# Kernel tuning notes

Hardware: AMD Instinct MI355X
Metric: run time of the kernel (lower is better)

Reference implementation:

```python
import math
import jax, jax.numpy as jnp
import numpy as np

SEQ, BATCH, D_MODEL, HEADS = 2048, 2, 1024, 16
D_K = D_MODEL // HEADS


def setup_inputs() -> dict:
    key = jax.random.key(0)
    ks = jax.random.split(key, 11)
    s = 1.0 / math.sqrt(D_MODEL)
    inp = {
        "q": jax.random.normal(ks[0], (SEQ, BATCH, D_MODEL), jnp.float32),
        "k": jax.random.normal(ks[1], (SEQ, BATCH, D_MODEL), jnp.float32),
        "v": jax.random.normal(ks[2], (SEQ, BATCH, D_MODEL), jnp.float32),
        "Wq": jax.random.normal(ks[3], (D_MODEL, D_MODEL), jnp.float32) * s,
        "bq": jnp.zeros((D_MODEL,), jnp.float32),
        "Wk": jax.random.normal(ks[4], (D_MODEL, D_MODEL), jnp.float32) * s,
        "bk": jnp.zeros((D_MODEL,), jnp.float32),
        "Wv": jax.random.normal(ks[5], (D_MODEL, D_MODEL), jnp.float32) * s,
        "bv": jnp.zeros((D_MODEL,), jnp.float32),
        "Wo": jax.random.normal(ks[6], (D_MODEL, D_MODEL), jnp.float32) * s,
        "bo": jnp.zeros((D_MODEL,), jnp.float32),
    }
    return inp


def _proj(x, W, b):
    # [S,B,D] @ [D, H*Dk] -> [S,B,H,Dk]
    y = jnp.einsum('sbd,de->sbe', x, W) + b
    return y.reshape(x.shape[0], x.shape[1], HEADS, D_K)


def reference(q, k, v, Wq, bq, Wk, bk, Wv, bv, Wo, bo):
    scale = 1.0 / math.sqrt(D_K)
    query = _proj(q, Wq, bq)            # [i,b,h,d]
    key_ = _proj(k, Wk, bk)             # [j,b,h,d]
    value = _proj(v, Wv, bv)            # [j,b,h,d]
    scores = jnp.einsum('ibhd,jbhd->ijbh', query, key_) * scale
    attn = jax.nn.softmax(scores, axis=1)  # softmax over key axis j (dim=1)
    x = jnp.einsum('ijbh,jbhd->ibhd', attn, value)
    x = x.reshape(SEQ, BATCH, D_MODEL)
    return jnp.einsum('sbd,de->sbe', x, Wo) + bo
```

## Files before the change

kernel.cpp:

```cpp
#include <hip/hip_runtime.h>
#include <hip/hip_bf16.h>


typedef __attribute__((ext_vector_type(8))) short bf16x8;
typedef __attribute__((ext_vector_type(4))) float f32x4;

constexpr int SEQ   = 2048;
constexpr int BATCH = 2;
constexpr int DM    = 1024;
constexpr int DK    = 64;
constexpr int MR    = SEQ * BATCH;
constexpr int SST   = BATCH * DM;
constexpr int HD    = SEQ * DK;

#define CE_SCALE 0.18033688011112042592f

__device__ __forceinline__ unsigned pkbf(float a, float b) {
    __hip_bfloat162 h = __float22bfloat162_rn(float2{a, b});
    union { __hip_bfloat162 h2; unsigned u; } cv;
    cv.h2 = h;
    return cv.u;
}

__device__ __forceinline__ f32x4 mfma16(bf16x8 a, bf16x8 b, f32x4 c) {
    return __builtin_amdgcn_mfma_f32_16x16x32_bf16(a, b, c, 0, 0, 0);
}

__device__ __forceinline__ void gl16(const unsigned short* g, unsigned short* l) {
    __builtin_amdgcn_global_load_lds(
        (const __attribute__((address_space(1))) void*)g,
        (__attribute__((address_space(3))) void*)l, 16, 0, 0);
}

__global__ __launch_bounds__(256)
void wt_prep_all(const float* __restrict__ w0, const float* __restrict__ w1,
                 const float* __restrict__ w2, const float* __restrict__ w3,
                 unsigned short* __restrict__ o0, unsigned short* __restrict__ o1,
                 unsigned short* __restrict__ o2, unsigned short* __restrict__ o3)
{
    const int z = blockIdx.z;
    const float* W = (z == 0) ? w0 : (z == 1) ? w1 : (z == 2) ? w2 : w3;
    unsigned short* Wt = (z == 0) ? o0 : (z == 1) ? o1 : (z == 2) ? o2 : o3;
    const float sc = (z == 0) ? CE_SCALE : 1.0f;

    const int t = threadIdx.x;
    const int e = blockIdx.x * 64 + (t & 63);
    const int dq = blockIdx.y * 256 + (t >> 6) * 64;
    unsigned short* orow = Wt + (size_t)e * DM + dq;
#pragma unroll
    for (int c = 0; c < 8; ++c) {
        float f[8];
#pragma unroll
        for (int j = 0; j < 8; ++j)
            f[j] = W[(size_t)(dq + c * 8 + j) * DM + e] * sc;
        uint4 u = { pkbf(f[0], f[1]), pkbf(f[2], f[3]),
                    pkbf(f[4], f[5]), pkbf(f[6], f[7]) };
        *(uint4*)(orow + c * 8) = u;
    }
}

__global__ __launch_bounds__(256)
void qkv_cast(const float* __restrict__ qa, const float* __restrict__ ka,
              const float* __restrict__ va,
              unsigned short* __restrict__ Qb, unsigned short* __restrict__ Kb,
              unsigned short* __restrict__ Vb)
{
    const int z = blockIdx.y;
    const float* src = (z == 0) ? qa : (z == 1) ? ka : va;
    unsigned short* dst = (z == 0) ? Qb : (z == 1) ? Kb : Vb;
    const size_t i = ((size_t)blockIdx.x * 256 + threadIdx.x) * 8;
    float4 f0 = *(const float4*)(src + i);
    float4 f1 = *(const float4*)(src + i + 4);
    uint4 u = { pkbf(f0.x, f0.y), pkbf(f0.z, f0.w),
                pkbf(f1.x, f1.y), pkbf(f1.z, f1.w) };
    *(uint4*)(dst + i) = u;
}

__global__ __launch_bounds__(512)
void qkv256(const unsigned short* __restrict__ Qb,
            const unsigned short* __restrict__ Kb,
            const unsigned short* __restrict__ Vb,
            const unsigned short* __restrict__ wq,
            const unsigned short* __restrict__ wk,
            const unsigned short* __restrict__ wv,
            const float* __restrict__ bq, const float* __restrict__ bk,
            const float* __restrict__ bv,
            unsigned short* __restrict__ Qh, unsigned short* __restrict__ Kh,
            unsigned short* __restrict__ Vtp)
{
    constexpr int K = 1024;
    constexpr int SLOT = 16384;
    __shared__ unsigned short smem[49152];

    const int z = blockIdx.y;
    const unsigned short* Ab = (z == 0) ? Qb : (z == 1) ? Kb : Vb;
    const unsigned short* Bt = (z == 0) ? wq : (z == 1) ? wk : wv;
    const float* bias = (z == 0) ? bq : (z == 1) ? bk : bv;
    const float bscale = (z == 0) ? CE_SCALE : 1.0f;

    const int bx = blockIdx.x;
    const int xcd = bx & 7, j64 = bx >> 3;
    const int bm = xcd * 2 + (j64 >> 2);
    const int bn = j64 & 3;

    const int tid = threadIdx.x;
    const int wave = tid >> 6, lane = tid & 63;
    const int wr = wave >> 2, wcn = wave & 3;
    const int lrow = lane & 15, g = lane >> 4;
    const int gr = lane & 15, gc = (lane >> 4) * 8;

    const unsigned short* aU0 = Ab + (size_t)(bm * 256 + wave * 32 + gr) * K + gc;
    const unsigned short* aU1 = aU0 + (size_t)16 * K;
    const unsigned short* bU0 = Bt + (size_t)(bn * 256 + wave * 32 + gr) * K + gc;
    const unsigned short* bU1 = bU0 + (size_t)16 * K;

    f32x4 acc[8][4] = {};

    auto stage = [&](int t, int slot) {
        unsigned short* As = smem + slot * SLOT;
        unsigned short* Bs = As + 8192;
        const int k0 = t * 32;
        gl16(aU0 + k0, As + (2 * wave) * 512);
        gl16(aU1 + k0, As + (2 * wave + 1) * 512);
        gl16(bU0 + k0, Bs + (2 * wave) * 512);
        gl16(bU1 + k0, Bs + (2 * wave + 1) * 512);
    };

    stage(0, 0);
    stage(1, 1);

    int bcur = 0;
#pragma unroll 1
    for (int t = 0; t < 32; ++t) {
        const unsigned short* As = smem + bcur * SLOT;
        const unsigned short* Bs = As + 8192;

        if (t < 31) { asm volatile("s_waitcnt vmcnt(4)" ::: "memory"); }
        else        { asm volatile("s_waitcnt vmcnt(0)" ::: "memory"); }
        __builtin_amdgcn_s_barrier();

        bf16x8 af[8], bfr[4];
#pragma unroll
        for (int i = 0; i < 8; ++i)
            af[i] = *(const bf16x8*)&As[(wr * 8 + i) * 512 + lane * 8];
#pragma unroll
        for (int j = 0; j < 4; ++j)
            bfr[j] = *(const bf16x8*)&Bs[(wcn * 4 + j) * 512 + lane * 8];
        asm volatile("s_waitcnt lgkmcnt(0)" ::: "memory");
        __builtin_amdgcn_sched_barrier(0);
        __builtin_amdgcn_s_barrier();

        if (t + 2 < 32) {
            int ns = bcur + 2; if (ns >= 3) ns -= 3;
            stage(t + 2, ns);
        }

        __builtin_amdgcn_s_setprio(1);
#pragma unroll
        for (int i = 0; i < 8; ++i)
#pragma unroll
            for (int j = 0; j < 4; ++j)
                acc[i][j] = mfma16(af[i], bfr[j], acc[i][j]);
        __builtin_amdgcn_s_setprio(0);

        bcur = (bcur + 1 == 3) ? 0 : bcur + 1;
    }

    constexpr int LBS = 258;
    __syncthreads();
#pragma unroll 1
    for (int rq = 0; rq < 4; ++rq) {
        if (wr == (rq >> 1)) {
            const int i0 = (rq & 1) * 4;
#pragma unroll
            for (int j = 0; j < 4; ++j) {
                const int c = wcn * 64 + j * 16 + lrow;
                const float bb = bias[bn * 256 + c] * bscale;
#pragma unroll
                for (int i2 = 0; i2 < 4; ++i2)
#pragma unroll
                    for (int r = 0; r < 4; ++r) {
                        const int lr = i2 * 16 + 4 * g + r;
                        smem[lr * LBS + c] =
                            (unsigned short)(pkbf(acc[i0 + i2][j][r] + bb, 0.f) & 0xffffu);
                    }
            }
        }
        __syncthreads();
        if (z != 2) {
            unsigned short* C = (z == 0) ? Qh : Kh;
            const int lr = tid >> 3, ch = (tid >> 1) & 3, hf = tid & 1;
            const int grow = bm * 256 + rq * 64 + lr;
            const int s = grow >> 1, b = grow & 1, h = bn * 4 + ch;
            const unsigned short* src = &smem[lr * LBS + ch * 64 + hf * 32];
            unsigned short* dst = C + (size_t)(b * 16 + h) * HD + (size_t)s * 64 + hf * 32;
#pragma unroll
            for (int w2 = 0; w2 < 4; ++w2)
                *(uint4*)(dst + w2 * 8) = *(const uint4*)(src + w2 * 8);
        } else {
            const int ch = tid >> 7, d = (tid >> 1) & 63, b = tid & 1;
            const int h = bn * 4 + ch;
            unsigned tmp[16];
#pragma unroll
            for (int m = 0; m < 16; ++m) {
                const int p0 = 2 * m, p1 = p0 + 1;
                const int r5a = ((p0 >> 2) & 1) * 16 + (p0 >> 3) * 4 + (p0 & 3);
                const int r5b = ((p1 >> 2) & 1) * 16 + (p1 >> 3) * 4 + (p1 & 3);
                const unsigned va  = smem[(2 * r5a + b) * LBS + ch * 64 + d];
                const unsigned vb2 = smem[(2 * r5b + b) * LBS + ch * 64 + d];
                tmp[m] = va | (vb2 << 16);
            }
            const int sbase = bm * 128 + rq * 32;
            const int st = sbase >> 6, kc = (sbase >> 5) & 1;
            unsigned short* dst = Vtp + (size_t)(b * 16 + h) * HD + (size_t)d * SEQ
                                      + st * 64 + kc * 32;
#pragma unroll
            for (int w2 = 0; w2 < 4; ++w2) {
                uint4 u = { tmp[4 * w2], tmp[4 * w2 + 1], tmp[4 * w2 + 2], tmp[4 * w2 + 3] };
                *(uint4*)(dst + w2 * 8) = u;
            }
        }
        __syncthreads();
    }
}

__global__ __launch_bounds__(256)
void attn_mfma(const unsigned short* __restrict__ Qh,
               const unsigned short* __restrict__ Kh,
               const unsigned short* __restrict__ Vtp,
               unsigned short* __restrict__ Xp)
{
    __shared__ unsigned short lds[24576];

    const int tid = threadIdx.x;
    const int fid = blockIdx.x;
    const int xcd = fid & 7, idx = fid >> 3;
    const int bh = xcd * 4 + (idx >> 4);
    const int qt = idx & 15;

    const int wave = tid >> 6, lane = tid & 63;
    const int lrow = lane & 15, g = lane >> 4;
    const int s7 = lrow & 7;
    const int q0w = qt * 128 + wave * 32;

    const unsigned short* qb = Qh + (size_t)bh * HD;
    const unsigned short* kb = Kh + (size_t)bh * HD;
    const unsigned short* vb = Vtp + (size_t)bh * HD;

    const int r8 = lane >> 3, c8 = lane & 7;
    const unsigned short* ksrcA = kb + (size_t)(wave * 16 + r8) * 64 + (c8 ^ r8) * 8;
    const unsigned short* ksrcB = ksrcA + 8 * 64;
    const unsigned short* vsrcA = vb + (size_t)(wave * 16 + r8) * SEQ + (c8 ^ r8) * 8;
    const unsigned short* vsrcB = vsrcA + 8 * SEQ;

    auto stage = [&](int t, unsigned short* base) {
        const size_t ko = (size_t)t * 4096;
        const size_t vo = (size_t)t * 64;
        gl16(ksrcA + ko, base + wave * 1024);
        gl16(ksrcB + ko, base + wave * 1024 + 512);
        gl16(vsrcA + vo, base + 4096 + wave * 1024);
        gl16(vsrcB + vo, base + 4096 + wave * 1024 + 512);
    };

    bf16x8 bq[2][2];
#pragma unroll
    for (int qi = 0; qi < 2; ++qi)
#pragma unroll
        for (int dc = 0; dc < 2; ++dc)
            bq[qi][dc] = *(const bf16x8*)(qb + (size_t)(q0w + qi * 16 + lrow) * 64
                                             + dc * 32 + g * 8);

    bf16x8 aones;
    {
        union { uint4 u; bf16x8 v; } cv;
        const unsigned o2 = (lrow == 0) ? 0x3F803F80u : 0u;
        cv.u = make_uint4(o2, o2, o2, o2);
        aones = cv.v;
    }

    f32x4 oacc[4][2] = {};
    f32x4 lacc[2] = {};

    const int off0 = lrow * 64 + ((g ^ s7) * 8);
    const int off1 = lrow * 64 + (((4 + g) ^ s7) * 8);

    stage(0, lds);
    stage(1, lds + 8192);

    int bcur = 0;
#pragma unroll 1
    for (int t = 0; t < 32; ++t) {
        unsigned short* kbuf = lds + bcur * 8192;
        unsigned short* vbuf = kbuf + 4096;

        if (t < 31) { asm volatile("s_waitcnt vmcnt(4)" ::: "memory"); }
        else        { asm volatile("s_waitcnt vmcnt(0)" ::: "memory"); }
        __builtin_amdgcn_s_barrier();

        bf16x8 ak[4][2], av[4][2];
#pragma unroll
        for (int kt = 0; kt < 4; ++kt) {
            ak[kt][0] = *(const bf16x8*)(kbuf + kt * 1024 + off0);
            ak[kt][1] = *(const bf16x8*)(kbuf + kt * 1024 + off1);
        }
#pragma unroll
        for (int dt = 0; dt < 4; ++dt) {
            av[dt][0] = *(const bf16x8*)(vbuf + dt * 1024 + off0);
            av[dt][1] = *(const bf16x8*)(vbuf + dt * 1024 + off1);
        }
        asm volatile("s_waitcnt lgkmcnt(0)" ::: "memory");
        __builtin_amdgcn_sched_barrier(0);
        __builtin_amdgcn_s_barrier();

        if (t + 2 < 32) {
            int bn3 = bcur + 2; if (bn3 >= 3) bn3 -= 3;
            stage(t + 2, lds + bn3 * 8192);
        }

        uint4 pbu[2][2];
        __builtin_amdgcn_s_setprio(1);
#pragma unroll
        for (int qi = 0; qi < 2; ++qi) {
#pragma unroll
            for (int kt = 0; kt < 4; ++kt) {
                f32x4 s = { 0.f, 0.f, 0.f, 0.f };
                s = mfma16(ak[kt][0], bq[qi][0], s);
                s = mfma16(ak[kt][1], bq[qi][1], s);
                const float p0 = __builtin_amdgcn_exp2f(s[0]);
                const float p1 = __builtin_amdgcn_exp2f(s[1]);
                const float p2 = __builtin_amdgcn_exp2f(s[2]);
                const float p3 = __builtin_amdgcn_exp2f(s[3]);
                const unsigned lo = pkbf(p0, p1);
                const unsigned hi = pkbf(p2, p3);
                if (kt & 1) { pbu[kt >> 1][qi].z = lo; pbu[kt >> 1][qi].w = hi; }
                else        { pbu[kt >> 1][qi].x = lo; pbu[kt >> 1][qi].y = hi; }
            }
        }

#pragma unroll
        for (int kc = 0; kc < 2; ++kc) {
#pragma unroll
            for (int dt = 0; dt < 4; ++dt)
#pragma unroll
                for (int qi = 0; qi < 2; ++qi) {
                    union { uint4 u; bf16x8 v; } cv;
                    cv.u = pbu[kc][qi];
                    oacc[dt][qi] = mfma16(av[dt][kc], cv.v, oacc[dt][qi]);
                }
#pragma unroll
            for (int qi = 0; qi < 2; ++qi) {
                union { uint4 u; bf16x8 v; } cv;
                cv.u = pbu[kc][qi];
                lacc[qi] = mfma16(aones, cv.v, lacc[qi]);
            }
        }
        __builtin_amdgcn_s_setprio(0);

        bcur = (bcur + 1 == 3) ? 0 : bcur + 1;
    }

    const float ls0 = __shfl(lacc[0][0], lrow);
    const float ls1 = __shfl(lacc[1][0], lrow);
    const float inv0 = 1.0f / ls0, inv1 = 1.0f / ls1;

    __builtin_amdgcn_s_barrier();

    unsigned short (*osh)[72] = (unsigned short (*)[72])(lds + wave * 32 * 72);
#pragma unroll
    for (int qi = 0; qi < 2; ++qi) {
        const float inv = qi ? inv1 : inv0;
#pragma unroll
        for (int dt = 0; dt < 4; ++dt) {
            const int d0 = dt * 16 + 4 * g;
            const unsigned u0 = pkbf(oacc[dt][qi][0] * inv, oacc[dt][qi][1] * inv);
            const unsigned u1 = pkbf(oacc[dt][qi][2] * inv, oacc[dt][qi][3] * inv);
            *(unsigned*)&osh[qi * 16 + lrow][d0] = u0;
            *(unsigned*)&osh[qi * 16 + lrow][d0 + 2] = u1;
        }
    }
    const int ql = lane >> 1;
    const int dh = (lane & 1) * 32;
    unsigned short* xrow = Xp + (size_t)(q0w + ql) * SST + bh * 64 + dh;
#pragma unroll
    for (int c = 0; c < 4; ++c) {
        uint4 vv = *(const uint4*)&osh[ql][dh + c * 8];
        *(uint4*)(xrow + c * 8) = vv;
    }
}

__global__ __launch_bounds__(256)
void gemm_out(const unsigned short* __restrict__ Xp,
              const unsigned short* __restrict__ WtO,
              const float* __restrict__ bias, float* __restrict__ out)
{
    constexpr int K = 1024, N = 1024;
    __shared__ unsigned short smem[12288];
    unsigned short* As0 = smem;
    unsigned short* As1 = smem + 4096;
    unsigned short* Bs0 = smem + 8192;
    unsigned short* Bs1 = smem + 10240;

    const int l = blockIdx.x + 16 * blockIdx.y;
    const int xcd = l & 7, jj0 = l >> 3;
    const int bm = xcd * 4 + (jj0 >> 4);
    const int bn = jj0 & 15;

    const int tid = threadIdx.x;
    const int wave = tid >> 6, lane = tid & 63;
    const int wr = wave >> 1, wc = wave & 1;
    const int lrow = lane & 15, g = lane >> 4;
    const int gr = lane & 15, gc = (lane >> 4) * 8;

    const unsigned short* aRow0 = Xp + (size_t)(bm * 128 + wave * 32 + gr) * K + gc;
    const unsigned short* aRow1 = aRow0 + (size_t)16 * K;
    const unsigned short* bRow0 = WtO + (size_t)(bn * 64 + wave * 16 + gr) * K + gc;

    f32x4 acc[4][2] = {};

    auto stage0 = [&](int k0) {
        gl16(aRow0 + k0, As0 + (2 * wave) * 512);
        gl16(aRow1 + k0, As0 + (2 * wave + 1) * 512);
        gl16(bRow0 + k0, Bs0 + wave * 512);
    };
    auto stage1 = [&](int k0) {
        gl16(aRow0 + k0, As1 + (2 * wave) * 512);
        gl16(aRow1 + k0, As1 + (2 * wave + 1) * 512);
        gl16(bRow0 + k0, Bs1 + wave * 512);
    };
    auto loadFrag = [&](bf16x8 (&af)[4], bf16x8 (&bfr)[2],
                        const unsigned short* as, const unsigned short* bs) {
#pragma unroll
        for (int i = 0; i < 4; ++i)
            af[i] = *(const bf16x8*)&as[(wr * 4 + i) * 512 + lane * 8];
#pragma unroll
        for (int j = 0; j < 2; ++j)
            bfr[j] = *(const bf16x8*)&bs[(wc * 2 + j) * 512 + lane * 8];
    };
    auto domfma = [&](bf16x8 (&af)[4], bf16x8 (&bfr)[2]) {
        __builtin_amdgcn_s_setprio(1);
#pragma unroll
        for (int i = 0; i < 4; ++i)
#pragma unroll
            for (int j = 0; j < 2; ++j)
                acc[i][j] = mfma16(af[i], bfr[j], acc[i][j]);
        __builtin_amdgcn_s_setprio(0);
    };

    stage0(0);
    stage1(32);

#pragma unroll 1
    for (int k0 = 0; k0 < 960; k0 += 64) {
        asm volatile("s_waitcnt vmcnt(3)" ::: "memory");
        __builtin_amdgcn_s_barrier();
        {
            bf16x8 af[4], bfr[2];
            loadFrag(af, bfr, As0, Bs0);
            asm volatile("s_waitcnt lgkmcnt(0)" ::: "memory");
            __builtin_amdgcn_sched_barrier(0);
            __builtin_amdgcn_s_barrier();
            stage0(k0 + 64);
            domfma(af, bfr);
        }
        asm volatile("s_waitcnt vmcnt(3)" ::: "memory");
        __builtin_amdgcn_s_barrier();
        {
            bf16x8 af[4], bfr[2];
            loadFrag(af, bfr, As1, Bs1);
            asm volatile("s_waitcnt lgkmcnt(0)" ::: "memory");
            __builtin_amdgcn_sched_barrier(0);
            __builtin_amdgcn_s_barrier();
            stage1(k0 + 96);
            domfma(af, bfr);
        }
    }
    {
        asm volatile("s_waitcnt vmcnt(3)" ::: "memory");
        __builtin_amdgcn_s_barrier();
        bf16x8 af[4], bfr[2];
        loadFrag(af, bfr, As0, Bs0);
        domfma(af, bfr);
    }
    {
        asm volatile("s_waitcnt vmcnt(0)" ::: "memory");
        __builtin_amdgcn_s_barrier();
        bf16x8 af[4], bfr[2];
        loadFrag(af, bfr, As1, Bs1);
        domfma(af, bfr);
    }

    __syncthreads();
    float* LF = (float*)smem;
#pragma unroll 1
    for (int q2 = 0; q2 < 2; ++q2) {
        if (wr == q2) {
#pragma unroll
            for (int j = 0; j < 2; ++j) {
                const int c = wc * 32 + j * 16 + lrow;
                const float bb = bias[bn * 64 + c];
#pragma unroll
                for (int i = 0; i < 4; ++i)
#pragma unroll
                    for (int r = 0; r < 4; ++r)
                        LF[(i * 16 + 4 * g + r) * 68 + c] = acc[i][j][r] + bb;
            }
        }
        __syncthreads();
        {
            const int lr = tid >> 2, c0 = (tid & 3) * 16;
            const float* srcp = &LF[lr * 68 + c0];
            float* dst = out + (size_t)(bm * 128 + q2 * 64 + lr) * N + bn * 64 + c0;
#pragma unroll
            for (int w2 = 0; w2 < 4; ++w2)
                *(float4*)(dst + w2 * 4) = *(const float4*)(srcp + w2 * 4);
        }
        __syncthreads();
    }
}

extern "C" void kernel_launch(void* const* d_in, const int* in_sizes, int n_in,
                              void* d_out, int out_size, void* d_ws, size_t ws_size,
                              hipStream_t stream) {
    (void)in_sizes; (void)n_in; (void)out_size; (void)ws_size;

    const float* q  = (const float*)d_in[0];
    const float* k  = (const float*)d_in[1];
    const float* v  = (const float*)d_in[2];
    const float* Wq = (const float*)d_in[3];
    const float* bq = (const float*)d_in[4];
    const float* Wk = (const float*)d_in[5];
    const float* bk = (const float*)d_in[6];
    const float* Wv = (const float*)d_in[7];
    const float* bv = (const float*)d_in[8];
    const float* Wo = (const float*)d_in[9];
    const float* bo = (const float*)d_in[10];
    float* out = (float*)d_out;

    unsigned short* ws = (unsigned short*)d_ws;
    const size_t WSZ = (size_t)DM * DM;
    const size_t MSZ = (size_t)MR * DM;
    unsigned short* WtQ = ws;
    unsigned short* WtK = ws + WSZ;
    unsigned short* WtV = ws + 2 * WSZ;
    unsigned short* WtO = ws + 3 * WSZ;
    unsigned short* Qb  = ws + 4 * WSZ;
    unsigned short* Kb  = Qb + MSZ;
    unsigned short* Vb  = Kb + MSZ;
    unsigned short* Qh  = Vb + MSZ;
    unsigned short* Kh  = Qh + MSZ;
    unsigned short* Vtp = Kh + MSZ;
    unsigned short* Xp  = Vtp + MSZ;

    wt_prep_all<<<dim3(16, 4, 4), dim3(256), 0, stream>>>(Wq, Wk, Wv, Wo,
                                                          WtQ, WtK, WtV, WtO);

    qkv_cast<<<dim3(2048, 3), dim3(256), 0, stream>>>(q, k, v, Qb, Kb, Vb);

    qkv256<<<dim3(64, 3), dim3(512), 0, stream>>>(Qb, Kb, Vb, WtQ, WtK, WtV,
                                                  bq, bk, bv, Qh, Kh, Vtp);

    attn_mfma<<<dim3(512), dim3(256), 0, stream>>>(Qh, Kh, Vtp, Xp);

    gemm_out<<<dim3(16, 32), dim3(256), 0, stream>>>(Xp, WtO, bo, out);
}
```

Before: 156.0 us.

## Fuse Q/K/V projections into one kernel with 128x128 tiles per block

Replaces the 3x64-block 256x256-tile projection GEMM with a single 256-block kernel where each 4-wave block computes a 128x128 tile for Q, K and V together, using double-buffered LDS slots of all six operand tiles. This aims to fill more CUs (256 blocks vs 192) and keep more MFMA work in flight per wave. It drops the triple-buffered pipeline for double buffering, lowers per-block reuse per operand (smaller tiles), and uses many more accumulator registers.

Result: faster. 152.4 us (-2.3%).

```diff
diff --git a/kernel.cpp b/kernel.cpp
--- a/kernel.cpp
+++ b/kernel.cpp
@@ -76,152 +76,164 @@
     *(uint4*)(dst + i) = u;
 }
 
-__global__ __launch_bounds__(512)
-void qkv256(const unsigned short* __restrict__ Qb,
-            const unsigned short* __restrict__ Kb,
-            const unsigned short* __restrict__ Vb,
-            const unsigned short* __restrict__ wq,
-            const unsigned short* __restrict__ wk,
-            const unsigned short* __restrict__ wv,
-            const float* __restrict__ bq, const float* __restrict__ bk,
-            const float* __restrict__ bv,
-            unsigned short* __restrict__ Qh, unsigned short* __restrict__ Kh,
-            unsigned short* __restrict__ Vtp)
+__global__ __launch_bounds__(256, 1)
+void qkv_fused(const unsigned short* __restrict__ Qb,
+               const unsigned short* __restrict__ Kb,
+               const unsigned short* __restrict__ Vb,
+               const unsigned short* __restrict__ wq,
+               const unsigned short* __restrict__ wk,
+               const unsigned short* __restrict__ wv,
+               const float* __restrict__ bq, const float* __restrict__ bk,
+               const float* __restrict__ bv,
+               unsigned short* __restrict__ Qh, unsigned short* __restrict__ Kh,
+               unsigned short* __restrict__ Vtp)
 {
     constexpr int K = 1024;
-    constexpr int SLOT = 16384;
+    constexpr int SLOT = 24576;
     __shared__ unsigned short smem[49152];
 
-    const int z = blockIdx.y;
-    const unsigned short* Ab = (z == 0) ? Qb : (z == 1) ? Kb : Vb;
-    const unsigned short* Bt = (z == 0) ? wq : (z == 1) ? wk : wv;
-    const float* bias = (z == 0) ? bq : (z == 1) ? bk : bv;
-    const float bscale = (z == 0) ? CE_SCALE : 1.0f;
-
-    const int bx = blockIdx.x;
-    const int xcd = bx & 7, j64 = bx >> 3;
-    const int bm = xcd * 2 + (j64 >> 2);
-    const int bn = j64 & 3;
+    const int l = blockIdx.x;
+    const int xcd = l & 7, jj = l >> 3;
+    const int bm = xcd * 4 + (jj >> 3);
+    const int bn = jj & 7;
 
     const int tid = threadIdx.x;
     const int wave = tid >> 6, lane = tid & 63;
-    const int wr = wave >> 2, wcn = wave & 3;
+    const int wr = wave >> 1, wc = wave & 1;
     const int lrow = lane & 15, g = lane >> 4;
     const int gr = lane & 15, gc = (lane >> 4) * 8;
 
-    const unsigned short* aU0 = Ab + (size_t)(bm * 256 + wave * 32 + gr) * K + gc;
-    const unsigned short* aU1 = aU0 + (size_t)16 * K;
-    const unsigned short* bU0 = Bt + (size_t)(bn * 256 + wave * 32 + gr) * K + gc;
-    const unsigned short* bU1 = bU0 + (size_t)16 * K;
-
-    f32x4 acc[8][4] = {};
+    const size_t aoff = (size_t)(bm * 128 + wave * 32 + gr) * K + gc;
+    const size_t boff = (size_t)(bn * 128 + wave * 32 + gr) * K + gc;
+    const unsigned short* aQ = Qb + aoff;
+    const unsigned short* aK = Kb + aoff;
+    const unsigned short* aV = Vb + aoff;
+    const unsigned short* bQ = wq + boff;
+    const unsigned short* bK = wk + boff;
+    const unsigned short* bV = wv + boff;
+    constexpr int ROW16 = 16 * 1024;
+
+    f32x4 accQ[4][4] = {}, accK[4][4] = {}, accV[4][4] = {};
 
     auto stage = [&](int t, int slot) {
-        unsigned short* As = smem + slot * SLOT;
-        unsigned short* Bs = As + 8192;
+        unsigned short* b = smem + slot * SLOT;
         const int k0 = t * 32;
-        gl16(aU0 + k0, As + (2 * wave) * 512);
-        gl16(aU1 + k0, As + (2 * wave + 1) * 512);
-        gl16(bU0 + k0, Bs + (2 * wave) * 512);
-        gl16(bU1 + k0, Bs + (2 * wave + 1) * 512);
+        const int g0 = (2 * wave) * 512, g1 = (2 * wave + 1) * 512;
+        gl16(aQ + k0,         b + g0);
+        gl16(aQ + ROW16 + k0, b + g1);
+        gl16(aK + k0,         b + 4096 + g0);
+        gl16(aK + ROW16 + k0, b + 4096 + g1);
+        gl16(aV + k0,         b + 8192 + g0);
+        gl16(aV + ROW16 + k0, b + 8192 + g1);
+        gl16(bQ + k0,         b + 12288 + g0);
+        gl16(bQ + ROW16 + k0, b + 12288 + g1);
+        gl16(bK + k0,         b + 16384 + g0);
+        gl16(bK + ROW16 + k0, b + 16384 + g1);
+        gl16(bV + k0,         b + 20480 + g0);
+        gl16(bV + ROW16 + k0, b + 20480 + g1);
     };
 
     stage(0, 0);
     stage(1, 1);
 
-    int bcur = 0;
 #pragma unroll 1
     for (int t = 0; t < 32; ++t) {
-        const unsigned short* As = smem + bcur * SLOT;
-        const unsigned short* Bs = As + 8192;
-
-        if (t < 31) { asm volatile("s_waitcnt vmcnt(4)" ::: "memory"); }
+        const unsigned short* base = smem + (t & 1) * SLOT;
+        if (t < 31) { asm volatile("s_waitcnt vmcnt(12)" ::: "memory"); }
         else        { asm volatile("s_waitcnt vmcnt(0)" ::: "memory"); }
         __builtin_amdgcn_s_barrier();
 
-        bf16x8 af[8], bfr[4];
-#pragma unroll
-        for (int i = 0; i < 8; ++i)
-            af[i] = *(const bf16x8*)&As[(wr * 8 + i) * 512 + lane * 8];
-#pragma unroll
-        for (int j = 0; j < 4; ++j)
-            bfr[j] = *(const bf16x8*)&Bs[(wcn * 4 + j) * 512 + lane * 8];
+        bf16x8 fAQ[4], fAK[4], fAV[4], fBQ[4], fBK[4], fBV[4];
+#pragma unroll
+        for (int i = 0; i < 4; ++i) {
+            const int ro = (wr * 4 + i) * 512 + lane * 8;
+            fAQ[i] = *(const bf16x8*)&base[ro];
+            fAK[i] = *(const bf16x8*)&base[4096 + ro];
+            fAV[i] = *(const bf16x8*)&base[8192 + ro];
+        }
+#pragma unroll
+        for (int j = 0; j < 4; ++j) {
+            const int co = (wc * 4 + j) * 512 + lane * 8;
+            fBQ[j] = *(const bf16x8*)&base[12288 + co];
+            fBK[j] = *(const bf16x8*)&base[16384 + co];
+            fBV[j] = *(const bf16x8*)&base[20480 + co];
+        }
         asm volatile("s_waitcnt lgkmcnt(0)" ::: "memory");
         __builtin_amdgcn_sched_barrier(0);
         __builtin_amdgcn_s_barrier();
 
-        if (t + 2 < 32) {
-            int ns = bcur + 2; if (ns >= 3) ns -= 3;
-            stage(t + 2, ns);
-        }
+        if (t + 2 < 32) stage(t + 2, t & 1);
 
         __builtin_amdgcn_s_setprio(1);
 #pragma unroll
-        for (int i = 0; i < 8; ++i)
-#pragma unroll
-            for (int j = 0; j < 4; ++j)
-                acc[i][j] = mfma16(af[i], bfr[j], acc[i][j]);
+        for (int i = 0; i < 4; ++i)
+#pragma unroll
+            for (int j = 0; j < 4; ++j) {
+                accQ[i][j] = mfma16(fAQ[i], fBQ[j], accQ[i][j]);
+                accK[i][j] = mfma16(fAK[i], fBK[j], accK[i][j]);
+                accV[i][j] = mfma16(fAV[i], fBV[j], accV[i][j]);
+            }
         __builtin_amdgcn_s_setprio(0);
-
-        bcur = (bcur + 1 == 3) ? 0 : bcur + 1;
-    }
-
-    constexpr int LBS = 258;
+    }
+
     __syncthreads();
+    auto epi = [&](const f32x4 (&acc)[4][4], const float* bias, float bscale,
+                   unsigned short* Cqh, bool isV) {
 #pragma unroll 1
-    for (int rq = 0; rq < 4; ++rq) {
-        if (wr == (rq >> 1)) {
-            const int i0 = (rq & 1) * 4;
-#pragma unroll
-            for (int j = 0; j < 4; ++j) {
-                const int c = wcn * 64 + j * 16 + lrow;
-                const float bb = bias[bn * 256 + c] * bscale;
-#pragma unroll
-                for (int i2 = 0; i2 < 4; ++i2)
-#pragma unroll
-                    for (int r = 0; r < 4; ++r) {
-                        const int lr = i2 * 16 + 4 * g + r;
-                        smem[lr * LBS + c] =
-                            (unsigned short)(pkbf(acc[i0 + i2][j][r] + bb, 0.f) & 0xffffu);
-                    }
+        for (int p = 0; p < 2; ++p) {
+            if (wc == p) {
+#pragma unroll
+                for (int j = 0; j < 4; ++j) {
+                    const int col = bn * 128 + p * 64 + j * 16 + lrow;
+                    const float bb = bias[col] * bscale;
+#pragma unroll
+                    for (int i = 0; i < 4; ++i)
+#pragma unroll
+                        for (int r = 0; r < 4; ++r) {
+                            const int lr = wr * 64 + i * 16 + 4 * g + r;
+                            smem[lr * 72 + j * 16 + lrow] =
+                                (unsigned short)(pkbf(acc[i][j][r] + bb, 0.f) & 0xffffu);
+                        }
+                }
             }
-        }
-        __syncthreads();
-        if (z != 2) {
-            unsigned short* C = (z == 0) ? Qh : Kh;
-            const int lr = tid >> 3, ch = (tid >> 1) & 3, hf = tid & 1;
-            const int grow = bm * 256 + rq * 64 + lr;
-            const int s = grow >> 1, b = grow & 1, h = bn * 4 + ch;
-            const unsigned short* src = &smem[lr * LBS + ch * 64 + hf * 32];
-            unsigned short* dst = C + (size_t)(b * 16 + h) * HD + (size_t)s * 64 + hf * 32;
-#pragma unroll
-            for (int w2 = 0; w2 < 4; ++w2)
-                *(uint4*)(dst + w2 * 8) = *(const uint4*)(src + w2 * 8);
-        } else {
-            const int ch = tid >> 7, d = (tid >> 1) & 63, b = tid & 1;
-            const int h = bn * 4 + ch;
-            unsigned tmp[16];
-#pragma unroll
-            for (int m = 0; m < 16; ++m) {
-                const int p0 = 2 * m, p1 = p0 + 1;
-                const int r5a = ((p0 >> 2) & 1) * 16 + (p0 >> 3) * 4 + (p0 & 3);
-                const int r5b = ((p1 >> 2) & 1) * 16 + (p1 >> 3) * 4 + (p1 & 3);
-                const unsigned va  = smem[(2 * r5a + b) * LBS + ch * 64 + d];
-                const unsigned vb2 = smem[(2 * r5b + b) * LBS + ch * 64 + d];
-                tmp[m] = va | (vb2 << 16);
+            __syncthreads();
+            if (!isV) {
+                const int lr = tid >> 1, half = tid & 1;
+                const int s = bm * 64 + (lr >> 1), b = lr & 1, h = bn * 2 + p;
+                const unsigned short* src = &smem[lr * 72 + half * 32];
+                unsigned short* dst = Cqh + (size_t)(b * 16 + h) * HD
+                                          + (size_t)s * 64 + half * 32;
+#pragma unroll
+                for (int w2 = 0; w2 < 4; ++w2)
+                    *(uint4*)(dst + w2 * 8) = *(const uint4*)(src + w2 * 8);
+            } else {
+                const int d = tid >> 2, b = (tid >> 1) & 1, sh = tid & 1;
+                const int h = bn * 2 + p;
+                unsigned tmp[16];
+#pragma unroll
+                for (int m = 0; m < 16; ++m) {
+                    const int p0 = 2 * m, p1 = p0 + 1;
+                    const int r5a = ((p0 >> 2) & 1) * 16 + (p0 >> 3) * 4 + (p0 & 3);
+                    const int r5b = ((p1 >> 2) & 1) * 16 + (p1 >> 3) * 4 + (p1 & 3);
+                    const unsigned va  = smem[(64 * sh + 2 * r5a + b) * 72 + d];
+                    const unsigned vb2 = smem[(64 * sh + 2 * r5b + b) * 72 + d];
+                    tmp[m] = va | (vb2 << 16);
+                }
+                unsigned short* dst = Vtp + (size_t)(b * 16 + h) * HD
+                                          + (size_t)d * SEQ + bm * 64 + sh * 32;
+#pragma unroll
+                for (int w2 = 0; w2 < 4; ++w2) {
+                    uint4 u = { tmp[4 * w2], tmp[4 * w2 + 1],
+                                tmp[4 * w2 + 2], tmp[4 * w2 + 3] };
+                    *(uint4*)(dst + w2 * 8) = u;
+                }
             }
-            const int sbase = bm * 128 + rq * 32;
-            const int st = sbase >> 6, kc = (sbase >> 5) & 1;
-            unsigned short* dst = Vtp + (size_t)(b * 16 + h) * HD + (size_t)d * SEQ
-                                      + st * 64 + kc * 32;
-#pragma unroll
-            for (int w2 = 0; w2 < 4; ++w2) {
-                uint4 u = { tmp[4 * w2], tmp[4 * w2 + 1], tmp[4 * w2 + 2], tmp[4 * w2 + 3] };
-                *(uint4*)(dst + w2 * 8) = u;
-            }
-        }
-        __syncthreads();
-    }
+            __syncthreads();
+        }
+    };
+    epi(accQ, bq, CE_SCALE, Qh, false);
+    epi(accK, bk, 1.0f, Kh, false);
+    epi(accV, bv, 1.0f, nullptr, true);
 }
 
 __global__ __launch_bounds__(256)
@@ -556,8 +568,8 @@
 
     qkv_cast<<<dim3(2048, 3), dim3(256), 0, stream>>>(q, k, v, Qb, Kb, Vb);
 
-    qkv256<<<dim3(64, 3), dim3(512), 0, stream>>>(Qb, Kb, Vb, WtQ, WtK, WtV,
-                                                  bq, bk, bv, Qh, Kh, Vtp);
+    qkv_fused<<<dim3(256), dim3(256), 0, stream>>>(Qb, Kb, Vb, WtQ, WtK, WtV,
+                                                   bq, bk, bv, Qh, Kh, Vtp);
 
     attn_mfma<<<dim3(512), dim3(256), 0, stream>>>(Qh, Kh, Vtp, Xp);
 
```
